# Optimization experiments

Hardware: AMD Instinct MI355X
Metric: run time of the kernel (lower is better)

## Reference

```python
import jax, jax.numpy as jnp
import numpy as np

HK, WK = 7, 11  # local_k


def _local_mask(H, W):
    # Equivalent to the torch buffer: 0 inside the hk x wk window centered on the
    # query position (for odd hk, wk), -inf outside. Shape (N, N), N = H*W.
    n = jnp.arange(H * W)
    hq, wq = n // W, n % W
    dh = jnp.abs(hq[:, None] - hq[None, :])
    dw = jnp.abs(wq[:, None] - wq[None, :])
    allowed = (dh <= HK // 2) & (dw <= WK // 2)
    return jnp.where(allowed, 0.0, -jnp.inf).astype(jnp.float32)


def setup_inputs() -> dict:
    key = jax.random.key(0)
    k1, k2, k3 = jax.random.split(key, 3)
    B, H, W, C = 8, 32, 64, 512
    N = H * W
    x = jax.random.normal(k1, (B, N, C), dtype=jnp.float32)
    qkv_w = jax.random.normal(k2, (3 * C, C), dtype=jnp.float32) * (C ** -0.5)
    proj_w = jax.random.normal(k3, (C, C), dtype=jnp.float32) * (C ** -0.5)
    proj_b = jnp.zeros((C,), dtype=jnp.float32)
    return {"x": x, "qkv_w": qkv_w, "proj_w": proj_w, "proj_b": proj_b, "H": H, "W": W}


def reference(x, qkv_w, proj_w, proj_b, H, W):
    B, N, C = x.shape
    num_heads = 8
    head_dim = C // num_heads
    scale = head_dim ** -0.5

    # qkv: Linear(dim, 3*dim, bias=False) -> (B, N, 3, heads, head_dim)
    qkv = (x @ qkv_w.T).reshape(B, N, 3, num_heads, head_dim)
    q = qkv[:, :, 0].transpose(0, 2, 1, 3) * scale  # (B, h, N, d)
    k = qkv[:, :, 1].transpose(0, 2, 1, 3)
    v = qkv[:, :, 2].transpose(0, 2, 1, 3)

    attn = jnp.einsum('bhnd,bhmd->bhnm', q, k)  # (B, h, N, N)
    attn = attn + _local_mask(H, W)  # broadcast over (B, h)
    attn = jax.nn.softmax(attn, axis=-1)

    out = jnp.einsum('bhnm,bhmd->bhnd', attn, v)  # (B, h, N, d)
    out = out.transpose(0, 2, 1, 3).reshape(B, N, C)
    return out @ proj_w.T + proj_b
```

## Files before the change

kernel.cpp:

```cpp
#include <hip/hip_runtime.h>
#include <hip/hip_bf16.h>

#define B_SZ 8
#define H_SZ 32
#define W_SZ 64
#define N_SZ 2048
#define C_SZ 512
#define NH 8
#define HD 64

using u16 = unsigned short;
typedef __attribute__((ext_vector_type(8))) short s16x8;
typedef __attribute__((ext_vector_type(4))) float f32x4;

__device__ __forceinline__ float bf2f(u16 u) {
    union { unsigned int i; float f; } c; c.i = ((unsigned int)u) << 16; return c.f;
}
__device__ __forceinline__ u16 f2bf(float f) {
    union { float f; unsigned int i; } c; c.f = f;
    unsigned int r = c.i + 0x7fffu + ((c.i >> 16) & 1u);
    return (u16)(r >> 16);
}

#define GLL16(gp, lp) __builtin_amdgcn_global_load_lds( \
    (const __attribute__((address_space(1))) unsigned int*)(gp), \
    (__attribute__((address_space(3))) unsigned int*)(lp), 16, 0, 0)

__device__ __forceinline__ int lds_off(int row, int chunk) {
    return (row * 8 + (chunk ^ (row & 7))) * 8;
}

#define NX4 2097152
#define NQ4 196608
#define NP4 65536
__global__ __launch_bounds__(256)
void conv_all(const float* __restrict__ x, const float* __restrict__ qw,
              const float* __restrict__ pw, u16* __restrict__ xb,
              u16* __restrict__ qwb, u16* __restrict__ pwb)
{
    const int i = blockIdx.x * 256 + threadIdx.x;
    const float* src; u16* dst; int idx; float sc = 1.0f;
    if (i < NX4)             { src = x;  dst = xb;  idx = i; }
    else if (i < NX4 + NQ4)  { src = qw; dst = qwb; idx = i - NX4;
                               if (idx < 65536) sc = 0.125f; }
    else                     { src = pw; dst = pwb; idx = i - NX4 - NQ4; }
    const float4 v = ((const float4*)src)[idx];
    ushort4 o = { f2bf(v.x * sc), f2bf(v.y * sc), f2bf(v.z * sc), f2bf(v.w * sc) };
    ((ushort4*)dst)[idx] = o;
}

template<int MODE, int NB>
__global__ __launch_bounds__(512, 2)
void gemm2(const u16* __restrict__ A, const u16* __restrict__ Bw,
           const float* __restrict__ bias,
           u16* __restrict__ q_ws, u16* __restrict__ k_ws, u16* __restrict__ v_ws,
           float* __restrict__ outp)
{
    __shared__ u16 As[2][256 * 64];
    __shared__ u16 Bs[2][128 * 64];
    const int t = threadIdx.x;
    const int chunk = gridDim.x >> 3;
    const int wg = (blockIdx.x & 7) * chunk + (blockIdx.x >> 3);
    const int m0 = (wg / NB) * 256;
    const int n0 = (wg % NB) * 128;
    const int wave = t >> 6, lane = t & 63;
    const int wm = (wave >> 1) * 64;
    const int wn = (wave & 1) * 64;
    const int l16 = lane & 15, quad = lane >> 4;
    const int srow = t >> 3;
    const int sch  = (t & 7) ^ (srow & 7);

    const u16* Ab = A  + (size_t)(m0 + srow) * C_SZ + sch * 8;
    const u16* Bb = Bw + (size_t)(n0 + srow) * C_SZ + sch * 8;

    f32x4 acc[4][4] = {};

    #pragma unroll
    for (int g = 0; g < 4; ++g)
        GLL16(Ab + (size_t)(64 * g) * C_SZ, &As[0][g * 4096 + t * 8]);
    #pragma unroll
    for (int g = 0; g < 2; ++g)
        GLL16(Bb + (size_t)(64 * g) * C_SZ, &Bs[0][g * 4096 + t * 8]);

    #pragma unroll
    for (int tt = 0; tt < 8; ++tt) {
        const int cur = tt & 1;
        if (tt < 7) {
            const int k0 = (tt + 1) * 64;
            #pragma unroll
            for (int g = 0; g < 4; ++g)
                GLL16(Ab + (size_t)(64 * g) * C_SZ + k0, &As[cur ^ 1][g * 4096 + t * 8]);
            #pragma unroll
            for (int g = 0; g < 2; ++g)
                GLL16(Bb + (size_t)(64 * g) * C_SZ + k0, &Bs[cur ^ 1][g * 4096 + t * 8]);
            asm volatile("s_waitcnt vmcnt(6)" ::: "memory");
        } else {
            asm volatile("s_waitcnt vmcnt(0)" ::: "memory");
        }
        __builtin_amdgcn_s_barrier();
        __builtin_amdgcn_sched_barrier(0);

        s16x8 af[4][2], bf[4][2];
        #pragma unroll
        for (int i = 0; i < 4; ++i) {
            const int R = wm + 16 * i + l16;
            af[i][0] = *(const s16x8*)&As[cur][lds_off(R, quad)];
            af[i][1] = *(const s16x8*)&As[cur][lds_off(R, 4 + quad)];
        }
        #pragma unroll
        for (int j = 0; j < 4; ++j) {
            const int R = wn + 16 * j + l16;
            bf[j][0] = *(const s16x8*)&Bs[cur][lds_off(R, quad)];
            bf[j][1] = *(const s16x8*)&Bs[cur][lds_off(R, 4 + quad)];
        }
        asm volatile("s_waitcnt lgkmcnt(0)" ::: "memory");
        __builtin_amdgcn_s_barrier();
        __builtin_amdgcn_sched_barrier(0);

        __builtin_amdgcn_s_setprio(1);
        #pragma unroll
        for (int i = 0; i < 4; ++i)
            #pragma unroll
            for (int j = 0; j < 4; ++j) {
                acc[i][j] = __builtin_amdgcn_mfma_f32_16x16x32_bf16(af[i][0], bf[j][0], acc[i][j], 0, 0, 0);
                acc[i][j] = __builtin_amdgcn_mfma_f32_16x16x32_bf16(af[i][1], bf[j][1], acc[i][j], 0, 0, 0);
            }
        __builtin_amdgcn_s_setprio(0);
    }

    if (MODE == 0) {
        const int bb  = m0 >> 11;
        const int nnb = (m0 & 2047) + wm + (quad << 2);
        if (n0 >= 1024) {
            #pragma unroll
            for (int j = 0; j < 4; ++j) {
                const int c  = n0 - 1024 + wn + 16 * j + l16;
                const int h  = c >> 6, dd = c & 63;
                u16* vp = v_ws + (((size_t)bb * NH + h) * HD + dd) * N_SZ + nnb;
                #pragma unroll
                for (int i = 0; i < 4; ++i) {
                    ushort4 st = { f2bf(acc[i][j][0]), f2bf(acc[i][j][1]),
                                   f2bf(acc[i][j][2]), f2bf(acc[i][j][3]) };
                    *(ushort4*)(vp + 16 * i) = st;
                }
            }
        } else {
            u16* T = (n0 < 512) ? q_ws : k_ws;
            const int nq = n0 & 511;
            #pragma unroll
            for (int j = 0; j < 4; ++j) {
                const int gn = nq + wn + 16 * j + l16;
                const int h  = gn >> 6, dd = gn & 63;
                u16* tp = T + (((size_t)bb * NH + h) * N_SZ + nnb) * HD + dd;
                #pragma unroll
                for (int i = 0; i < 4; ++i)
                    #pragma unroll
                    for (int r = 0; r < 4; ++r)
                        tp[(size_t)(16 * i + r) * HD] = f2bf(acc[i][j][r]);
            }
        }
    } else {
        #pragma unroll
        for (int j = 0; j < 4; ++j) {
            const int gn = n0 + wn + 16 * j + l16;
            const float bv = bias[gn];
            #pragma unroll
            for (int i = 0; i < 4; ++i)
                #pragma unroll
                for (int r = 0; r < 4; ++r)
                    outp[(size_t)(m0 + wm + 16 * i + (quad << 2) + r) * C_SZ + gn]
                        = acc[i][j][r] + bv;
        }
    }
}

__global__ __launch_bounds__(256)
void attn_mfma(const u16* __restrict__ q_ws, const u16* __restrict__ k_ws,
               const u16* __restrict__ vt_ws, u16* __restrict__ o_ws)
{
    __shared__ u16 KV[2][64 * 64];
    __shared__ u16 Ps[4][16 * 40];

    const int t = threadIdx.x, wave = t >> 6, lane = t & 63;
    const int l16 = lane & 15, quad = lane >> 4;
    const int u  = blockIdx.x;
    const int p  = u & 15;
    const int bh = u >> 4;
    const int r0 = 2 * p, r1 = 2 * p + 1;
    const size_t base = (size_t)bh * (N_SZ * HD);
    const int srow = t >> 3;
    const int sch  = (t & 7) ^ (srow & 7);

    const u16* qg = q_ws + base + (size_t)r0 * (64 * HD);
    u16* Qst = &KV[0][0];
    #pragma unroll
    for (int g = 0; g < 4; ++g)
        GLL16(qg + (size_t)(srow + 32 * g) * 64 + sch * 8, Qst + g * 2048 + t * 8);
    __syncthreads();

    s16x8 aQ[2][2];
    #pragma unroll
    for (int s = 0; s < 2; ++s) {
        const int Rq = 64 * s + 16 * wave + l16;
        aQ[s][0] = *(const s16x8*)&Qst[lds_off(Rq, quad)];
        aQ[s][1] = *(const s16x8*)&Qst[lds_off(Rq, 4 + quad)];
    }

    const int kb = min(max(16 * wave - 8, 0), 32);

    f32x4 accO[2][4] = {};
    float lp[2][4] = {};

    const int hlo = (r0 - 3 < 0) ? 0 : r0 - 3;
    const int hhi = (r1 + 3 > H_SZ - 1) ? H_SZ - 1 : r1 + 3;

    for (int hh = hlo; hh <= hhi; ++hh) {
        __syncthreads();
        const u16* kg = k_ws + base + (size_t)hh * (64 * HD);
        GLL16(kg + (size_t)srow        * 64 + sch * 8, &KV[0][t * 8]);
        GLL16(kg + (size_t)(srow + 32) * 64 + sch * 8, &KV[0][2048 + t * 8]);
        const u16* vg = vt_ws + base + (size_t)hh * 64;
        GLL16(vg + (size_t)srow        * N_SZ + sch * 8, &KV[1][t * 8]);
        GLL16(vg + (size_t)(srow + 32) * N_SZ + sch * 8, &KV[1][2048 + t * 8]);
        __syncthreads();

        s16x8 bK[2][2];
        #pragma unroll
        for (int j = 0; j < 2; ++j) {
            const int Rk = kb + 16 * j + l16;
            bK[j][0] = *(const s16x8*)&KV[0][lds_off(Rk, quad)];
            bK[j][1] = *(const s16x8*)&KV[0][lds_off(Rk, 4 + quad)];
        }
        s16x8 vf[4];
        #pragma unroll
        for (int j = 0; j < 4; ++j)
            vf[j] = *(const s16x8*)&KV[1][lds_off(16 * j + l16, (kb >> 3) + quad)];

        #pragma unroll
        for (int s = 0; s < 2; ++s) {
            const int dh = hh - (r0 + s);
            if (dh * dh > 9) continue;
            f32x4 z[2] = {{0.f,0.f,0.f,0.f},{0.f,0.f,0.f,0.f}};
            #pragma unroll
            for (int j = 0; j < 2; ++j) {
                z[j] = __builtin_amdgcn_mfma_f32_16x16x32_bf16(aQ[s][0], bK[j][0], z[j], 0, 0, 0);
                z[j] = __builtin_amdgcn_mfma_f32_16x16x32_bf16(aQ[s][1], bK[j][1], z[j], 0, 0, 0);
            }
            #pragma unroll
            for (int j = 0; j < 2; ++j) {
                const int ww = kb + 16 * j + l16;
                #pragma unroll
                for (int r = 0; r < 4; ++r) {
                    const int dw = ww - (16 * wave + quad * 4 + r);
                    const float pv = (dw * dw <= 25) ? __expf(z[j][r]) : 0.f;
                    const u16 pb = f2bf(pv);
                    lp[s][r] += bf2f(pb);
                    Ps[wave][(quad * 4 + r) * 40 + 16 * j + l16] = pb;
                }
            }
            s16x8 aP = *(const s16x8*)&Ps[wave][l16 * 40 + quad * 8];
            #pragma unroll
            for (int j = 0; j < 4; ++j)
                accO[s][j] = __builtin_amdgcn_mfma_f32_16x16x32_bf16(aP, vf[j], accO[s][j], 0, 0, 0);
        }
    }

    #pragma unroll
    for (int s = 0; s < 2; ++s)
        #pragma unroll
        for (int r = 0; r < 4; ++r) {
            lp[s][r] += __shfl_xor(lp[s][r], 1);
            lp[s][r] += __shfl_xor(lp[s][r], 2);
            lp[s][r] += __shfl_xor(lp[s][r], 4);
            lp[s][r] += __shfl_xor(lp[s][r], 8);
        }

    const int bb = bh >> 3, h = bh & 7;
    #pragma unroll
    for (int s = 0; s < 2; ++s)
        #pragma unroll
        for (int j = 0; j < 4; ++j)
            #pragma unroll
            for (int r = 0; r < 4; ++r) {
                const int row = (r0 + s) * 64 + 16 * wave + quad * 4 + r;
                o_ws[((size_t)bb * N_SZ + row) * C_SZ + h * 64 + 16 * j + l16]
                    = f2bf(accO[s][j][r] / lp[s][r]);
            }
}

extern "C" void kernel_launch(void* const* d_in, const int* in_sizes, int n_in,
                              void* d_out, int out_size, void* d_ws, size_t ws_size,
                              hipStream_t stream)
{
    const float* x      = (const float*)d_in[0];
    const float* qkv_w  = (const float*)d_in[1];
    const float* proj_w = (const float*)d_in[2];
    const float* proj_b = (const float*)d_in[3];
    float* outp = (float*)d_out;

    const size_t seg = (size_t)B_SZ * NH * N_SZ * HD;
    u16* q_ws = (u16*)d_ws;
    u16* k_ws = q_ws + seg;
    u16* v_ws = k_ws + seg;
    u16* o_ws = v_ws + seg;
    u16* xb   = o_ws + seg;
    u16* qwb  = xb + (size_t)16384 * 512;
    u16* pwb  = qwb + (size_t)1536 * 512;

    conv_all<<<9216, 256, 0, stream>>>(x, qkv_w, proj_w, xb, qwb, pwb);

    gemm2<0, 12><<<768, 512, 0, stream>>>(xb, qwb, nullptr,
                                          q_ws, k_ws, v_ws, nullptr);
    attn_mfma<<<B_SZ * NH * (H_SZ / 2), 256, 0, stream>>>(q_ws, k_ws, v_ws, o_ws);
    gemm2<1, 4><<<256, 512, 0, stream>>>(o_ws, pwb, proj_b,
                                         nullptr, nullptr, nullptr, outp);
}
```

Before: 174.0 us.

## Split GEMM k-step into two phases, interleaving B-fragment LDS reads with MFMAs

The bf16 GEMM mainloop now loads A fragments and only half of the B fragments first, then issues the next tile's global-to-LDS prefetch. It computes the first half of the MFMAs, then reads the remaining B fragments and computes the second half, with an extra barrier between the phases. The aim is to overlap LDS reads with matrix work and shorten the LDS-read stall before each MFMA burst. The cost is that the prefetch is issued later in each iteration and has to fully drain at the next step, plus an extra workgroup barrier per k-step.

```diff
diff --git a/kernel.cpp b/kernel.cpp
--- a/kernel.cpp
+++ b/kernel.cpp
@@ -85,22 +85,11 @@
     #pragma unroll
     for (int tt = 0; tt < 8; ++tt) {
         const int cur = tt & 1;
-        if (tt < 7) {
-            const int k0 = (tt + 1) * 64;
-            #pragma unroll
-            for (int g = 0; g < 4; ++g)
-                GLL16(Ab + (size_t)(64 * g) * C_SZ + k0, &As[cur ^ 1][g * 4096 + t * 8]);
-            #pragma unroll
-            for (int g = 0; g < 2; ++g)
-                GLL16(Bb + (size_t)(64 * g) * C_SZ + k0, &Bs[cur ^ 1][g * 4096 + t * 8]);
-            asm volatile("s_waitcnt vmcnt(6)" ::: "memory");
-        } else {
-            asm volatile("s_waitcnt vmcnt(0)" ::: "memory");
-        }
+        asm volatile("s_waitcnt vmcnt(0)" ::: "memory");
         __builtin_amdgcn_s_barrier();
         __builtin_amdgcn_sched_barrier(0);
 
-        s16x8 af[4][2], bf[4][2];
+        s16x8 af[4][2], bf0[2][2];
         #pragma unroll
         for (int i = 0; i < 4; ++i) {
             const int R = wm + 16 * i + l16;
@@ -108,12 +97,21 @@
             af[i][1] = *(const s16x8*)&As[cur][lds_off(R, 4 + quad)];
         }
         #pragma unroll
-        for (int j = 0; j < 4; ++j) {
+        for (int j = 0; j < 2; ++j) {
             const int R = wn + 16 * j + l16;
-            bf[j][0] = *(const s16x8*)&Bs[cur][lds_off(R, quad)];
-            bf[j][1] = *(const s16x8*)&Bs[cur][lds_off(R, 4 + quad)];
-        }
-        asm volatile("s_waitcnt lgkmcnt(0)" ::: "memory");
+            bf0[j][0] = *(const s16x8*)&Bs[cur][lds_off(R, quad)];
+            bf0[j][1] = *(const s16x8*)&Bs[cur][lds_off(R, 4 + quad)];
+        }
+        if (tt < 7) {
+            const int k0 = (tt + 1) * 64;
+            #pragma unroll
+            for (int g = 0; g < 4; ++g)
+                GLL16(Ab + (size_t)(64 * g) * C_SZ + k0, &As[cur ^ 1][g * 4096 + t * 8]);
+            #pragma unroll
+            for (int g = 0; g < 2; ++g)
+                GLL16(Bb + (size_t)(64 * g) * C_SZ + k0, &Bs[cur ^ 1][g * 4096 + t * 8]);
+        }
+        __builtin_amdgcn_sched_barrier(0);
         __builtin_amdgcn_s_barrier();
         __builtin_amdgcn_sched_barrier(0);
 
@@ -121,11 +119,33 @@
         #pragma unroll
         for (int i = 0; i < 4; ++i)
             #pragma unroll
-            for (int j = 0; j < 4; ++j) {
-                acc[i][j] = __builtin_amdgcn_mfma_f32_16x16x32_bf16(af[i][0], bf[j][0], acc[i][j], 0, 0, 0);
-                acc[i][j] = __builtin_amdgcn_mfma_f32_16x16x32_bf16(af[i][1], bf[j][1], acc[i][j], 0, 0, 0);
+            for (int j = 0; j < 2; ++j) {
+                acc[i][j] = __builtin_amdgcn_mfma_f32_16x16x32_bf16(af[i][0], bf0[j][0], acc[i][j], 0, 0, 0);
+                acc[i][j] = __builtin_amdgcn_mfma_f32_16x16x32_bf16(af[i][1], bf0[j][1], acc[i][j], 0, 0, 0);
             }
         __builtin_amdgcn_s_setprio(0);
+
+        s16x8 bf1[2][2];
+        #pragma unroll
+        for (int j = 0; j < 2; ++j) {
+            const int R = wn + 32 + 16 * j + l16;
+            bf1[j][0] = *(const s16x8*)&Bs[cur][lds_off(R, quad)];
+            bf1[j][1] = *(const s16x8*)&Bs[cur][lds_off(R, 4 + quad)];
+        }
+        __builtin_amdgcn_sched_barrier(0);
+        __builtin_amdgcn_s_barrier();
+        __builtin_amdgcn_sched_barrier(0);
+
+        __builtin_amdgcn_s_setprio(1);
+        #pragma unroll
+        for (int i = 0; i < 4; ++i)
+            #pragma unroll
+            for (int j = 0; j < 2; ++j) {
+                acc[i][2 + j] = __builtin_amdgcn_mfma_f32_16x16x32_bf16(af[i][0], bf1[j][0], acc[i][2 + j], 0, 0, 0);
+                acc[i][2 + j] = __builtin_amdgcn_mfma_f32_16x16x32_bf16(af[i][1], bf1[j][1], acc[i][2 + j], 0, 0, 0);
+            }
+        __builtin_amdgcn_s_setprio(0);
+        __builtin_amdgcn_sched_barrier(0);
     }
 
     if (MODE == 0) {
```

Result: slower. 177.6 us (+2.0%).

## Restructure GEMM to triple-buffered K=32 stages with 2x4 wave layout

Applied to the files above, without the earlier changes.

The GEMM kernel now stages K in 32-wide slices with a three-deep LDS ring buffer instead of two 64-wide buffers. This cuts LDS use enough to allow four blocks per CU and drops one barrier per iteration. The wave tiling changes from 4x2 (64x64 per wave) to 2x4 (128x32 per wave), and each wave's A loads are split into two halves interleaved with MFMA groups. In exchange there are twice as many iterations with smaller MFMA batches per sync, more A-fragment LDS reads relative to B, and a scattered epilogue with more rows per wave.

```diff
diff --git a/kernel.cpp b/kernel.cpp
--- a/kernel.cpp
+++ b/kernel.cpp
@@ -28,6 +28,9 @@
 
 __device__ __forceinline__ int lds_off(int row, int chunk) {
     return (row * 8 + (chunk ^ (row & 7))) * 8;
+}
+__device__ __forceinline__ int lds_off32(int row, int chunk) {
+    return (row * 4 + (chunk ^ (row & 3))) * 8;
 }
 
 #define NX4 2097152
@@ -50,81 +53,83 @@
 }
 
 template<int MODE, int NB>
-__global__ __launch_bounds__(512, 2)
-void gemm2(const u16* __restrict__ A, const u16* __restrict__ Bw,
+__global__ __launch_bounds__(512, 4)
+void gemm3(const u16* __restrict__ A, const u16* __restrict__ Bw,
            const float* __restrict__ bias,
            u16* __restrict__ q_ws, u16* __restrict__ k_ws, u16* __restrict__ v_ws,
            float* __restrict__ outp)
 {
-    __shared__ u16 As[2][256 * 64];
-    __shared__ u16 Bs[2][128 * 64];
+    __shared__ u16 As[3][256 * 32];
+    __shared__ u16 Bs[3][128 * 32];
     const int t = threadIdx.x;
     const int chunk = gridDim.x >> 3;
     const int wg = (blockIdx.x & 7) * chunk + (blockIdx.x >> 3);
     const int m0 = (wg / NB) * 256;
     const int n0 = (wg % NB) * 128;
     const int wave = t >> 6, lane = t & 63;
-    const int wm = (wave >> 1) * 64;
-    const int wn = (wave & 1) * 64;
+    const int wm = (wave >> 2) * 128;
+    const int wn = (wave & 3) * 32;
     const int l16 = lane & 15, quad = lane >> 4;
-    const int srow = t >> 3;
-    const int sch  = (t & 7) ^ (srow & 7);
+    const int srow = t >> 2;
+    const int sch  = (t & 3) ^ (srow & 3);
 
     const u16* Ab = A  + (size_t)(m0 + srow) * C_SZ + sch * 8;
     const u16* Bb = Bw + (size_t)(n0 + srow) * C_SZ + sch * 8;
 
-    f32x4 acc[4][4] = {};
-
-    #pragma unroll
-    for (int g = 0; g < 4; ++g)
-        GLL16(Ab + (size_t)(64 * g) * C_SZ, &As[0][g * 4096 + t * 8]);
-    #pragma unroll
-    for (int g = 0; g < 2; ++g)
-        GLL16(Bb + (size_t)(64 * g) * C_SZ, &Bs[0][g * 4096 + t * 8]);
-
-    #pragma unroll
-    for (int tt = 0; tt < 8; ++tt) {
-        const int cur = tt & 1;
-        if (tt < 7) {
-            const int k0 = (tt + 1) * 64;
-            #pragma unroll
-            for (int g = 0; g < 4; ++g)
-                GLL16(Ab + (size_t)(64 * g) * C_SZ + k0, &As[cur ^ 1][g * 4096 + t * 8]);
-            #pragma unroll
-            for (int g = 0; g < 2; ++g)
-                GLL16(Bb + (size_t)(64 * g) * C_SZ + k0, &Bs[cur ^ 1][g * 4096 + t * 8]);
-            asm volatile("s_waitcnt vmcnt(6)" ::: "memory");
-        } else {
-            asm volatile("s_waitcnt vmcnt(0)" ::: "memory");
-        }
+    f32x4 acc[8][2] = {};
+
+    #pragma unroll
+    for (int tb = 0; tb < 2; ++tb) {
+        GLL16(Ab + tb * 32,                       &As[tb][t * 8]);
+        GLL16(Ab + (size_t)128 * C_SZ + tb * 32,  &As[tb][4096 + t * 8]);
+        GLL16(Bb + tb * 32,                       &Bs[tb][t * 8]);
+    }
+
+    #pragma unroll
+    for (int tt = 0; tt < 16; ++tt) {
+        const int cb = tt % 3;
+        if (tt < 15) asm volatile("s_waitcnt vmcnt(3)" ::: "memory");
+        else         asm volatile("s_waitcnt vmcnt(0)" ::: "memory");
         __builtin_amdgcn_s_barrier();
         __builtin_amdgcn_sched_barrier(0);
 
-        s16x8 af[4][2], bf[4][2];
-        #pragma unroll
-        for (int i = 0; i < 4; ++i) {
-            const int R = wm + 16 * i + l16;
-            af[i][0] = *(const s16x8*)&As[cur][lds_off(R, quad)];
-            af[i][1] = *(const s16x8*)&As[cur][lds_off(R, 4 + quad)];
-        }
-        #pragma unroll
-        for (int j = 0; j < 4; ++j) {
-            const int R = wn + 16 * j + l16;
-            bf[j][0] = *(const s16x8*)&Bs[cur][lds_off(R, quad)];
-            bf[j][1] = *(const s16x8*)&Bs[cur][lds_off(R, 4 + quad)];
-        }
+        if (tt < 14) {
+            const int nb = (tt + 2) % 3;
+            const int k0 = (tt + 2) * 32;
+            GLL16(Ab + k0,                         &As[nb][t * 8]);
+            GLL16(Ab + (size_t)128 * C_SZ + k0,    &As[nb][4096 + t * 8]);
+            GLL16(Bb + k0,                         &Bs[nb][t * 8]);
+        }
+
+        s16x8 af0[4], bf[2];
+        #pragma unroll
+        for (int i = 0; i < 4; ++i)
+            af0[i] = *(const s16x8*)&As[cb][lds_off32(wm + 16 * i + l16, quad)];
+        #pragma unroll
+        for (int j = 0; j < 2; ++j)
+            bf[j] = *(const s16x8*)&Bs[cb][lds_off32(wn + 16 * j + l16, quad)];
         asm volatile("s_waitcnt lgkmcnt(0)" ::: "memory");
-        __builtin_amdgcn_s_barrier();
         __builtin_amdgcn_sched_barrier(0);
-
         __builtin_amdgcn_s_setprio(1);
         #pragma unroll
         for (int i = 0; i < 4; ++i)
             #pragma unroll
-            for (int j = 0; j < 4; ++j) {
-                acc[i][j] = __builtin_amdgcn_mfma_f32_16x16x32_bf16(af[i][0], bf[j][0], acc[i][j], 0, 0, 0);
-                acc[i][j] = __builtin_amdgcn_mfma_f32_16x16x32_bf16(af[i][1], bf[j][1], acc[i][j], 0, 0, 0);
-            }
+            for (int j = 0; j < 2; ++j)
+                acc[i][j] = __builtin_amdgcn_mfma_f32_16x16x32_bf16(af0[i], bf[j], acc[i][j], 0, 0, 0);
+        __builtin_amdgcn_s_setprio(0);
+
+        s16x8 af1[4];
+        #pragma unroll
+        for (int i = 0; i < 4; ++i)
+            af1[i] = *(const s16x8*)&As[cb][lds_off32(wm + 64 + 16 * i + l16, quad)];
+        asm volatile("s_waitcnt lgkmcnt(0)" ::: "memory");
+        __builtin_amdgcn_sched_barrier(0);
+        __builtin_amdgcn_s_setprio(1);
+        #pragma unroll
+        for (int i = 0; i < 4; ++i)
+            #pragma unroll
+            for (int j = 0; j < 2; ++j)
+                acc[4 + i][j] = __builtin_amdgcn_mfma_f32_16x16x32_bf16(af1[i], bf[j], acc[4 + i][j], 0, 0, 0);
         __builtin_amdgcn_s_setprio(0);
     }
 
@@ -133,12 +138,12 @@
         const int nnb = (m0 & 2047) + wm + (quad << 2);
         if (n0 >= 1024) {
             #pragma unroll
-            for (int j = 0; j < 4; ++j) {
+            for (int j = 0; j < 2; ++j) {
                 const int c  = n0 - 1024 + wn + 16 * j + l16;
                 const int h  = c >> 6, dd = c & 63;
                 u16* vp = v_ws + (((size_t)bb * NH + h) * HD + dd) * N_SZ + nnb;
                 #pragma unroll
-                for (int i = 0; i < 4; ++i) {
+                for (int i = 0; i < 8; ++i) {
                     ushort4 st = { f2bf(acc[i][j][0]), f2bf(acc[i][j][1]),
                                    f2bf(acc[i][j][2]), f2bf(acc[i][j][3]) };
                     *(ushort4*)(vp + 16 * i) = st;
@@ -148,12 +153,12 @@
             u16* T = (n0 < 512) ? q_ws : k_ws;
             const int nq = n0 & 511;
             #pragma unroll
-            for (int j = 0; j < 4; ++j) {
+            for (int j = 0; j < 2; ++j) {
                 const int gn = nq + wn + 16 * j + l16;
                 const int h  = gn >> 6, dd = gn & 63;
                 u16* tp = T + (((size_t)bb * NH + h) * N_SZ + nnb) * HD + dd;
                 #pragma unroll
-                for (int i = 0; i < 4; ++i)
+                for (int i = 0; i < 8; ++i)
                     #pragma unroll
                     for (int r = 0; r < 4; ++r)
                         tp[(size_t)(16 * i + r) * HD] = f2bf(acc[i][j][r]);
@@ -161,11 +166,11 @@
         }
     } else {
         #pragma unroll
-        for (int j = 0; j < 4; ++j) {
+        for (int j = 0; j < 2; ++j) {
             const int gn = n0 + wn + 16 * j + l16;
             const float bv = bias[gn];
             #pragma unroll
-            for (int i = 0; i < 4; ++i)
+            for (int i = 0; i < 8; ++i)
                 #pragma unroll
                 for (int r = 0; r < 4; ++r)
                     outp[(size_t)(m0 + wm + 16 * i + (quad << 2) + r) * C_SZ + gn]
@@ -309,9 +314,9 @@
 
     conv_all<<<9216, 256, 0, stream>>>(x, qkv_w, proj_w, xb, qwb, pwb);
 
-    gemm2<0, 12><<<768, 512, 0, stream>>>(xb, qwb, nullptr,
+    gemm3<0, 12><<<768, 512, 0, stream>>>(xb, qwb, nullptr,
                                           q_ws, k_ws, v_ws, nullptr);
     attn_mfma<<<B_SZ * NH * (H_SZ / 2), 256, 0, stream>>>(q_ws, k_ws, v_ws, o_ws);
-    gemm2<1, 4><<<256, 512, 0, stream>>>(o_ws, pwb, proj_b,
+    gemm3<1, 4><<<256, 512, 0, stream>>>(o_ws, pwb, proj_b,
                                          nullptr, nullptr, nullptr, outp);
 }
```

Measured after the change: 177.7 us. 1.02x slower.

## Retile GEMM to 128x256 with triple-buffered LDS and interleaved prefetch

Applied to the files above, without the earlier changes.

Changes the GEMM block tile from 256x128 to 128x256 with a 2x4 wave layout. It replaces double buffering with a three-stage LDS ring that prefetches two k-steps ahead. Global loads for the next stage are split across two halves of the MFMA work so memory traffic overlaps compute, and the second barrier per iteration is dropped. LDS use rises to about 144KB per block, which removes the two-blocks-per-CU occupancy hint and may reduce latency hiding.

```diff
diff --git a/kernel.cpp b/kernel.cpp
--- a/kernel.cpp
+++ b/kernel.cpp
@@ -50,22 +50,22 @@
 }
 
 template<int MODE, int NB>
-__global__ __launch_bounds__(512, 2)
-void gemm2(const u16* __restrict__ A, const u16* __restrict__ Bw,
+__global__ __launch_bounds__(512)
+void gemm8(const u16* __restrict__ A, const u16* __restrict__ Bw,
            const float* __restrict__ bias,
            u16* __restrict__ q_ws, u16* __restrict__ k_ws, u16* __restrict__ v_ws,
            float* __restrict__ outp)
 {
-    __shared__ u16 As[2][256 * 64];
-    __shared__ u16 Bs[2][128 * 64];
+    __shared__ u16 As[3][128 * 64];
+    __shared__ u16 Bs[3][256 * 64];
     const int t = threadIdx.x;
     const int chunk = gridDim.x >> 3;
     const int wg = (blockIdx.x & 7) * chunk + (blockIdx.x >> 3);
-    const int m0 = (wg / NB) * 256;
-    const int n0 = (wg % NB) * 128;
+    const int m0 = (wg / NB) * 128;
+    const int n0 = (wg % NB) * 256;
     const int wave = t >> 6, lane = t & 63;
-    const int wm = (wave >> 1) * 64;
-    const int wn = (wave & 1) * 64;
+    const int wm = (wave >> 2) * 64;
+    const int wn = (wave & 3) * 64;
     const int l16 = lane & 15, quad = lane >> 4;
     const int srow = t >> 3;
     const int sch  = (t & 7) ^ (srow & 7);
@@ -75,58 +75,75 @@
 
     f32x4 acc[4][4] = {};
 
-    #pragma unroll
-    for (int g = 0; g < 4; ++g)
-        GLL16(Ab + (size_t)(64 * g) * C_SZ, &As[0][g * 4096 + t * 8]);
-    #pragma unroll
-    for (int g = 0; g < 2; ++g)
-        GLL16(Bb + (size_t)(64 * g) * C_SZ, &Bs[0][g * 4096 + t * 8]);
+#define STAGE_Ag(b, k0, g) GLL16(Ab + (size_t)(64 * (g)) * C_SZ + (k0), \
+                                 &As[b][(g) * 4096 + t * 8])
+#define STAGE_Bg(b, k0, g) GLL16(Bb + (size_t)(64 * (g)) * C_SZ + (k0), \
+                                 &Bs[b][(g) * 4096 + t * 8])
+
+    #pragma unroll
+    for (int tb = 0; tb < 2; ++tb) {
+        STAGE_Ag(tb, tb * 64, 0); STAGE_Ag(tb, tb * 64, 1);
+        STAGE_Bg(tb, tb * 64, 0); STAGE_Bg(tb, tb * 64, 1);
+        STAGE_Bg(tb, tb * 64, 2); STAGE_Bg(tb, tb * 64, 3);
+    }
 
     #pragma unroll
     for (int tt = 0; tt < 8; ++tt) {
-        const int cur = tt & 1;
-        if (tt < 7) {
-            const int k0 = (tt + 1) * 64;
-            #pragma unroll
-            for (int g = 0; g < 4; ++g)
-                GLL16(Ab + (size_t)(64 * g) * C_SZ + k0, &As[cur ^ 1][g * 4096 + t * 8]);
-            #pragma unroll
-            for (int g = 0; g < 2; ++g)
-                GLL16(Bb + (size_t)(64 * g) * C_SZ + k0, &Bs[cur ^ 1][g * 4096 + t * 8]);
-            asm volatile("s_waitcnt vmcnt(6)" ::: "memory");
-        } else {
-            asm volatile("s_waitcnt vmcnt(0)" ::: "memory");
-        }
+        const int cb = tt % 3;
+        const int nb = (tt + 2) % 3;
+        const int k2 = (tt + 2) * 64;
+        if (tt < 7) asm volatile("s_waitcnt vmcnt(6)" ::: "memory");
+        else        asm volatile("s_waitcnt vmcnt(0)" ::: "memory");
         __builtin_amdgcn_s_barrier();
         __builtin_amdgcn_sched_barrier(0);
 
-        s16x8 af[4][2], bf[4][2];
-        #pragma unroll
-        for (int i = 0; i < 4; ++i) {
+        s16x8 af0[2][2], bf[4][2];
+        #pragma unroll
+        for (int i = 0; i < 2; ++i) {
             const int R = wm + 16 * i + l16;
-            af[i][0] = *(const s16x8*)&As[cur][lds_off(R, quad)];
-            af[i][1] = *(const s16x8*)&As[cur][lds_off(R, 4 + quad)];
+            af0[i][0] = *(const s16x8*)&As[cb][lds_off(R, quad)];
+            af0[i][1] = *(const s16x8*)&As[cb][lds_off(R, 4 + quad)];
         }
         #pragma unroll
         for (int j = 0; j < 4; ++j) {
             const int R = wn + 16 * j + l16;
-            bf[j][0] = *(const s16x8*)&Bs[cur][lds_off(R, quad)];
-            bf[j][1] = *(const s16x8*)&Bs[cur][lds_off(R, 4 + quad)];
-        }
-        asm volatile("s_waitcnt lgkmcnt(0)" ::: "memory");
-        __builtin_amdgcn_s_barrier();
+            bf[j][0] = *(const s16x8*)&Bs[cb][lds_off(R, quad)];
+            bf[j][1] = *(const s16x8*)&Bs[cb][lds_off(R, 4 + quad)];
+        }
+        if (tt < 6) { STAGE_Ag(nb, k2, 0); STAGE_Ag(nb, k2, 1); STAGE_Bg(nb, k2, 0); }
         __builtin_amdgcn_sched_barrier(0);
-
         __builtin_amdgcn_s_setprio(1);
         #pragma unroll
-        for (int i = 0; i < 4; ++i)
+        for (int i = 0; i < 2; ++i)
             #pragma unroll
             for (int j = 0; j < 4; ++j) {
-                acc[i][j] = __builtin_amdgcn_mfma_f32_16x16x32_bf16(af[i][0], bf[j][0], acc[i][j], 0, 0, 0);
-                acc[i][j] = __builtin_amdgcn_mfma_f32_16x16x32_bf16(af[i][1], bf[j][1], acc[i][j], 0, 0, 0);
+                acc[i][j] = __builtin_amdgcn_mfma_f32_16x16x32_bf16(af0[i][0], bf[j][0], acc[i][j], 0, 0, 0);
+                acc[i][j] = __builtin_amdgcn_mfma_f32_16x16x32_bf16(af0[i][1], bf[j][1], acc[i][j], 0, 0, 0);
             }
         __builtin_amdgcn_s_setprio(0);
-    }
+
+        s16x8 af1[2][2];
+        #pragma unroll
+        for (int i = 0; i < 2; ++i) {
+            const int R = wm + 32 + 16 * i + l16;
+            af1[i][0] = *(const s16x8*)&As[cb][lds_off(R, quad)];
+            af1[i][1] = *(const s16x8*)&As[cb][lds_off(R, 4 + quad)];
+        }
+        if (tt < 6) { STAGE_Bg(nb, k2, 1); STAGE_Bg(nb, k2, 2); STAGE_Bg(nb, k2, 3); }
+        __builtin_amdgcn_sched_barrier(0);
+        __builtin_amdgcn_s_setprio(1);
+        #pragma unroll
+        for (int i = 0; i < 2; ++i)
+            #pragma unroll
+            for (int j = 0; j < 4; ++j) {
+                acc[2 + i][j] = __builtin_amdgcn_mfma_f32_16x16x32_bf16(af1[i][0], bf[j][0], acc[2 + i][j], 0, 0, 0);
+                acc[2 + i][j] = __builtin_amdgcn_mfma_f32_16x16x32_bf16(af1[i][1], bf[j][1], acc[2 + i][j], 0, 0, 0);
+            }
+        __builtin_amdgcn_s_setprio(0);
+        __builtin_amdgcn_sched_barrier(0);
+    }
+#undef STAGE_Ag
+#undef STAGE_Bg
 
     if (MODE == 0) {
         const int bb  = m0 >> 11;
@@ -150,7 +167,7 @@
             #pragma unroll
             for (int j = 0; j < 4; ++j) {
                 const int gn = nq + wn + 16 * j + l16;
-                const int h  = gn >> 6, dd = gn & 63;
+                const int h  = (gn >> 6) & 7, dd = gn & 63;
                 u16* tp = T + (((size_t)bb * NH + h) * N_SZ + nnb) * HD + dd;
                 #pragma unroll
                 for (int i = 0; i < 4; ++i)
@@ -309,9 +326,9 @@
 
     conv_all<<<9216, 256, 0, stream>>>(x, qkv_w, proj_w, xb, qwb, pwb);
 
-    gemm2<0, 12><<<768, 512, 0, stream>>>(xb, qwb, nullptr,
-                                          q_ws, k_ws, v_ws, nullptr);
+    gemm8<0, 6><<<768, 512, 0, stream>>>(xb, qwb, nullptr,
+                                         q_ws, k_ws, v_ws, nullptr);
     attn_mfma<<<B_SZ * NH * (H_SZ / 2), 256, 0, stream>>>(q_ws, k_ws, v_ws, o_ws);
-    gemm2<1, 4><<<256, 512, 0, stream>>>(o_ws, pwb, proj_b,
+    gemm8<1, 2><<<256, 512, 0, stream>>>(o_ws, pwb, proj_b,
                                          nullptr, nullptr, nullptr, outp);
 }
```

Result: no change. 173.9 us (-0.1%).
